# Optimization experiments

Hardware: AMD Instinct MI355X
Metric: run time of the kernel (lower is better)

## Reference

```python
import jax, jax.numpy as jnp
import numpy as np

N = 32768      # total nodes
E = 524288     # edges (avg degree 16)
HID = 256      # hidden_dim
H = 8          # heads
C = HID // H   # head dim = 32
G = 64         # graphs in batch
NPG = N // G   # nodes per graph = 512
EDIM = 2       # edge feature dim
NEG_SLOPE = 0.2  # PyG GATv2 default


def setup_inputs():
    key = jax.random.key(0)
    ks = jax.random.split(key, 12)
    s = 0.05
    return dict(
        x=jax.random.normal(ks[0], (N, HID), jnp.float32),
        edge_attr=jax.random.normal(ks[1], (E, EDIM), jnp.float32),
        # GATv2Conv params
        W_l=jax.random.normal(ks[2], (HID, HID), jnp.float32) * s,
        b_l=jnp.zeros((HID,), jnp.float32),
        W_r=jax.random.normal(ks[3], (HID, HID), jnp.float32) * s,
        b_r=jnp.zeros((HID,), jnp.float32),
        W_e=jax.random.normal(ks[4], (EDIM, HID), jnp.float32) * s,
        att=jax.random.normal(ks[5], (H, C), jnp.float32) * s,
        bias_gat=jnp.zeros((HID,), jnp.float32),
        # MultiheadAttention params (torch packed qkv layout)
        in_proj_w=jax.random.normal(ks[6], (3 * HID, HID), jnp.float32) * s,
        in_proj_b=jnp.zeros((3 * HID,), jnp.float32),
        out_proj_w=jax.random.normal(ks[7], (HID, HID), jnp.float32) * s,
        out_proj_b=jnp.zeros((HID,), jnp.float32),
        alpha_param=jnp.array(0.5, jnp.float32),
        # FFN
        W1=jax.random.normal(ks[8], (HID, 4 * HID), jnp.float32) * s,
        b1=jnp.zeros((4 * HID,), jnp.float32),
        W2=jax.random.normal(ks[9], (4 * HID, HID), jnp.float32) * s,
        b2=jnp.zeros((HID,), jnp.float32),
        # LayerNorms
        g1=jnp.ones((HID,), jnp.float32), be1=jnp.zeros((HID,), jnp.float32),
        g2=jnp.ones((HID,), jnp.float32), be2=jnp.zeros((HID,), jnp.float32),
        g3=jnp.ones((HID,), jnp.float32), be3=jnp.zeros((HID,), jnp.float32),
        edge_index=jax.random.randint(ks[10], (2, E), 0, N, jnp.int32),
        batch=jnp.repeat(jnp.arange(G, dtype=jnp.int32), NPG),
    )


def _ln(x, g, b, eps=1e-5):
    m = jnp.mean(x, -1, keepdims=True)
    v = jnp.mean((x - m) ** 2, -1, keepdims=True)
    return (x - m) * jax.lax.rsqrt(v + eps) * g + b


def _gatv2(x, edge_index, edge_attr, W_l, b_l, W_r, b_r, W_e, att, bias_gat):
    src, dst = edge_index[0], edge_index[1]
    # PyG add_self_loops with fill_value='mean': self-loop edge_attr at node i
    # is the mean of edge_attr over edges incoming to i (0 if none).
    deg = jax.ops.segment_sum(jnp.ones((E,), x.dtype), dst, num_segments=N)
    ea_mean = jax.ops.segment_sum(edge_attr, dst, num_segments=N) / jnp.maximum(deg, 1.0)[:, None]
    loop = jnp.arange(N, dtype=src.dtype)
    src2 = jnp.concatenate([src, loop])
    dst2 = jnp.concatenate([dst, loop])
    ea2 = jnp.concatenate([edge_attr, ea_mean], axis=0)  # [E+N, 2]
    xl = (x @ W_l + b_l).reshape(N, H, C)  # source transform (messages)
    xr = (x @ W_r + b_r).reshape(N, H, C)  # target transform
    ee = (ea2 @ W_e).reshape(-1, H, C)
    e = jax.nn.leaky_relu(xl[src2] + xr[dst2] + ee, NEG_SLOPE)  # [E+N, H, C]
    score = jnp.einsum('ehc,hc->eh', e, att)  # [E+N, H]
    # scatter softmax over incoming edges of each target node
    smax = jax.lax.stop_gradient(jax.ops.segment_max(score, dst2, num_segments=N))
    ex = jnp.exp(score - smax[dst2])
    ssum = jax.ops.segment_sum(ex, dst2, num_segments=N)
    alpha = ex / ssum[dst2]  # [E+N, H]
    out = jax.ops.segment_sum(alpha[:, :, None] * xl[src2], dst2, num_segments=N)
    return out.reshape(N, HID) + bias_gat


def _mha(xg, in_proj_w, in_proj_b, out_proj_w, out_proj_b):
    # xg: [G, NPG, HID]; torch nn.MultiheadAttention (batch_first, eval mode)
    qkv = xg @ in_proj_w.T + in_proj_b
    q, k, v = jnp.split(qkv, 3, axis=-1)
    q = q.reshape(G, NPG, H, C)
    k = k.reshape(G, NPG, H, C)
    v = v.reshape(G, NPG, H, C)
    scores = jnp.einsum('gqhd,gkhd->ghqk', q, k) / jnp.sqrt(jnp.float32(C))
    p = jax.nn.softmax(scores, axis=-1)
    o = jnp.einsum('ghqk,gkhd->gqhd', p, v).reshape(G, NPG, HID)
    return o @ out_proj_w.T + out_proj_b


def reference(x, edge_attr, W_l, b_l, W_r, b_r, W_e, att, bias_gat,
              in_proj_w, in_proj_b, out_proj_w, out_proj_b, alpha_param,
              W1, b1, W2, b2, g1, be1, g2, be2, g3, be3, edge_index, batch):
    local_out = _ln(
        _gatv2(x, edge_index, edge_attr, W_l, b_l, W_r, b_r, W_e, att, bias_gat),
        g1, be1)
    # batch is sorted with equal-sized graphs -> the per-graph ragged
    # attention loop equals one batched [G, NPG, NPG] attention
    xg = x.reshape(G, NPG, HID)
    global_out = _mha(xg, in_proj_w, in_proj_b, out_proj_w, out_proj_b).reshape(N, HID)
    global_out = _ln(global_out, g2, be2)
    a = jax.nn.sigmoid(alpha_param)
    combined = a * local_out + (1.0 - a) * global_out
    ffn = jax.nn.gelu(combined @ W1 + b1, approximate=False) @ W2 + b2
    return _ln(combined + ffn, g3, be3)
```

## Files before the change

kernel.cpp:

```cpp
#include <hip/hip_runtime.h>
#include <math.h>

#define N_NODES 32768
#define E_EDGES 524288
#define HIDDEN  256
#define NPG     512
#define NGRAPH  64
#define NHEAD   8
#define CDIM    32

typedef unsigned short bf16;
typedef __attribute__((ext_vector_type(8))) short short8;
typedef __attribute__((ext_vector_type(4))) float f4;

#define AS1 __attribute__((address_space(1)))
#define AS3 __attribute__((address_space(3)))

__device__ __forceinline__ void cp16(const bf16* g, bf16* l) {
    __builtin_amdgcn_global_load_lds((AS1 const unsigned int*)(const void*)g,
                                     (AS3 unsigned int*)(void*)l, 16, 0, 0);
}

__device__ inline float bf2f(unsigned short u) {
    union { unsigned int i; float f; } v; v.i = ((unsigned int)u) << 16; return v.f;
}
__device__ inline unsigned short f2bf(float f) {
    union { float f; unsigned int i; } v; v.f = f;
    unsigned int x = v.i;
    return (unsigned short)((x + 0x7FFFu + ((x >> 16) & 1u)) >> 16);
}
__device__ inline unsigned short f2bf_trunc(float f) {
    return (unsigned short)(__float_as_uint(f) >> 16);
}
__device__ inline float4 load4(const float* p) { return *(const float4*)p; }
__device__ inline float4 load4(const bf16* p) {
    ushort4 u = *(const ushort4*)p;
    return make_float4(bf2f(u.x), bf2f(u.y), bf2f(u.z), bf2f(u.w));
}
__device__ inline void store4(float* p, float4 v) { *(float4*)p = v; }
__device__ inline void store4(bf16* p, float4 v) {
    ushort4 u; u.x = f2bf(v.x); u.y = f2bf(v.y); u.z = f2bf(v.z); u.w = f2bf(v.w);
    *(ushort4*)p = u;
}


__global__ void zero_kernel(float* deg, float* ea_sum, int* fill) {
    int i = blockIdx.x * blockDim.x + threadIdx.x;
    if (i < 2 * N_NODES) ea_sum[i] = 0.0f;
    if (i < N_NODES) { deg[i] = 0.0f; fill[i] = 0; }
}

__global__ void deg_kernel(const int* __restrict__ ei, const float* __restrict__ edge_attr,
                           float* deg, float* ea_sum) {
    int e = blockIdx.x * blockDim.x + threadIdx.x;
    if (e >= E_EDGES) return;
    int d = ei[E_EDGES + e];
    atomicAdd(&deg[d], 1.0f);
    atomicAdd(&ea_sum[2 * d + 0], edge_attr[2 * e + 0]);
    atomicAdd(&ea_sum[2 * d + 1], edge_attr[2 * e + 1]);
}

__global__ __launch_bounds__(1024) void scan_kernel(const float* __restrict__ deg, int* row_ptr) {
    __shared__ int part[1024];
    int t = threadIdx.x;
    int base = t * 32;
    int loc[32];
    int s = 0;
    #pragma unroll
    for (int j = 0; j < 32; j++) {
        loc[j] = s;
        s += (int)deg[base + j] + 1;
    }
    int mysum = s;
    part[t] = s;
    __syncthreads();
    for (int off = 1; off < 1024; off <<= 1) {
        int v = 0;
        if (t >= off) v = part[t - off];
        __syncthreads();
        part[t] += v;
        __syncthreads();
    }
    int offset = part[t] - mysum;
    #pragma unroll
    for (int j = 0; j < 32; j++) row_ptr[base + j] = offset + loc[j];
    if (t == 1023) row_ptr[N_NODES] = part[1023];
}

__global__ void fill_kernel(const int* __restrict__ ei, const float* __restrict__ edge_attr,
                            const float* __restrict__ ea_sum, const float* __restrict__ deg,
                            const int* __restrict__ row_ptr, int* fill, int4* __restrict__ erec) {
    int tid = blockIdx.x * blockDim.x + threadIdx.x;
    if (tid >= E_EDGES + N_NODES) return;
    int d, src; float a0, a1;
    if (tid < E_EDGES) {
        d = ei[E_EDGES + tid];
        src = ei[tid];
        a0 = edge_attr[2 * tid + 0];
        a1 = edge_attr[2 * tid + 1];
    } else {
        d = tid - E_EDGES;
        src = d;
        float dm = fmaxf(deg[d], 1.0f);
        a0 = ea_sum[2 * d + 0] / dm;
        a1 = ea_sum[2 * d + 1] / dm;
    }
    int pos = row_ptr[d] + atomicAdd(&fill[d], 1);
    int4 r;
    r.x = src;
    r.y = __float_as_int(a0);
    r.z = __float_as_int(a1);
    r.w = 0;
    erec[pos] = r;
}

#define QSCALE 0.25506882685716462f
__global__ void convall(const float* __restrict__ x,
                        const float* __restrict__ W_l, const float* __restrict__ W_r,
                        const float* __restrict__ W1, const float* __restrict__ W2,
                        const float* __restrict__ in_proj_w, const float* __restrict__ out_proj_w,
                        const float* __restrict__ b_l, const float* __restrict__ b_r,
                        const float* __restrict__ in_proj_b,
                        bf16* xb, bf16* wlrb, bf16* w1b, bf16* w2b,
                        bf16* wipb, bf16* wopb, float* blr, float* ipb2)
{
    int b = blockIdx.x, t = threadIdx.x;
    if (b < 8192) {
        int i = b * 256 + t;
        store4(&xb[i * 4], *(const float4*)&x[i * 4]);
    } else if (b < 8448) {
        int i = (b - 8192) * 256 + t; int k = i >> 8, n = i & 255;
        wlrb[n * 256 + k] = f2bf(W_l[i]);
    } else if (b < 8704) {
        int i = (b - 8448) * 256 + t; int k = i >> 8, n = i & 255;
        wlrb[(256 + n) * 256 + k] = f2bf(W_r[i]);
    } else if (b < 9728) {
        int i = (b - 8704) * 256 + t; int k = i >> 10, n = i & 1023;
        w1b[n * 256 + k] = f2bf(W1[i]);
    } else if (b < 10752) {
        int i = (b - 9728) * 256 + t; int k = i >> 8, n = i & 255;
        w2b[n * 1024 + k] = f2bf(W2[i]);
    } else if (b < 10944) {
        int i = (b - 10752) * 256 + t;
        float4 v = *(const float4*)&in_proj_w[i * 4];
        if (i < 16384) { v.x *= QSCALE; v.y *= QSCALE; v.z *= QSCALE; v.w *= QSCALE; }
        store4(&wipb[i * 4], v);
    } else if (b < 11008) {
        int i = (b - 10944) * 256 + t;
        store4(&wopb[i * 4], *(const float4*)&out_proj_w[i * 4]);
    } else {
        blr[t] = b_l[t]; blr[256 + t] = b_r[t];
        ipb2[t] = in_proj_b[t] * QSCALE;
        ipb2[256 + t] = in_proj_b[256 + t];
        ipb2[512 + t] = in_proj_b[512 + t];
    }
}

template <int EPI>
__global__ __launch_bounds__(256) void mfma_gemm(
    const bf16* __restrict__ A, const bf16* __restrict__ Wb,
    const float* __restrict__ bias, const bf16* __restrict__ res,
    bf16* __restrict__ C, int M, int N, int K)
{
    __shared__ bf16 lds[2 * 128 * 64];
    bf16* As = lds;
    bf16* Bs = lds + 128 * 64;
    int tid = threadIdx.x;
    int wave = tid >> 6, lane = tid & 63;
    int quad = lane >> 4, l16 = lane & 15;
    int n0 = blockIdx.x * 128, m0 = blockIdx.y * 128;
    int wm = (wave & 1) * 64, wn = (wave >> 1) * 64;

    f4 acc[4][4] = {};
    int srow = tid >> 3;
    int scol = (tid & 7) * 8;

    for (int k0 = 0; k0 < K; k0 += 64) {
        #pragma unroll
        for (int i = 0; i < 4; i++) {
            int row = i * 32 + srow;
            cp16(&A[(size_t)(m0 + row) * K + k0 + scol], &As[row * 64 + scol]);
            cp16(&Wb[(size_t)(n0 + row) * K + k0 + scol], &Bs[row * 64 + scol]);
        }
        __syncthreads();
        #pragma unroll
        for (int ks = 0; ks < 2; ks++) {
            short8 af[4], bfr[4];
            #pragma unroll
            for (int mt = 0; mt < 4; mt++)
                af[mt] = *(const short8*)&As[(wm + mt * 16 + l16) * 64 + ks * 32 + quad * 8];
            #pragma unroll
            for (int nt = 0; nt < 4; nt++)
                bfr[nt] = *(const short8*)&Bs[(wn + nt * 16 + l16) * 64 + ks * 32 + quad * 8];
            #pragma unroll
            for (int mt = 0; mt < 4; mt++)
                #pragma unroll
                for (int nt = 0; nt < 4; nt++)
                    acc[mt][nt] = __builtin_amdgcn_mfma_f32_16x16x32_bf16(
                        af[mt], bfr[nt], acc[mt][nt], 0, 0, 0);
        }
        __syncthreads();
    }

    float* epi = (float*)lds + wave * 16 * 68;
    int row = lane >> 2;
    int cb = (lane & 3) * 16;
    int gn = n0 + wn + cb;
    float bb[16];
    *(float4*)&bb[0]  = *(const float4*)&bias[gn + 0];
    *(float4*)&bb[4]  = *(const float4*)&bias[gn + 4];
    *(float4*)&bb[8]  = *(const float4*)&bias[gn + 8];
    *(float4*)&bb[12] = *(const float4*)&bias[gn + 12];

    for (int mt = 0; mt < 4; mt++) {
        #pragma unroll
        for (int nt = 0; nt < 4; nt++)
            #pragma unroll
            for (int r = 0; r < 4; r++)
                epi[(quad * 4 + r) * 68 + nt * 16 + l16] = acc[mt][nt][r];
        float vv[16];
        *(float4*)&vv[0]  = *(float4*)&epi[row * 68 + cb + 0];
        *(float4*)&vv[4]  = *(float4*)&epi[row * 68 + cb + 4];
        *(float4*)&vv[8]  = *(float4*)&epi[row * 68 + cb + 8];
        *(float4*)&vv[12] = *(float4*)&epi[row * 68 + cb + 12];
        int gm = m0 + wm + mt * 16 + row;
        #pragma unroll
        for (int j = 0; j < 16; j++) vv[j] += bb[j];
        if (EPI == 1) {
            #pragma unroll
            for (int j = 0; j < 16; j++)
                vv[j] = 0.5f * vv[j] * (1.0f + erff(vv[j] * 0.70710678118654752f));
        } else if (EPI == 4) {
            ushort rr[16];
            const bf16* rp = &res[(size_t)gm * N + gn];
            *(int4*)&rr[0] = *(const int4*)&rp[0];
            *(int4*)&rr[8] = *(const int4*)&rp[8];
            #pragma unroll
            for (int j = 0; j < 16; j++) vv[j] += bf2f(rr[j]);
            float* cf = (float*)C + (size_t)gm * N + gn;
            *(float4*)&cf[0]  = *(float4*)&vv[0];
            *(float4*)&cf[4]  = *(float4*)&vv[4];
            *(float4*)&cf[8]  = *(float4*)&vv[8];
            *(float4*)&cf[12] = *(float4*)&vv[12];
            continue;
        }
        ushort o16[16];
        #pragma unroll
        for (int j = 0; j < 16; j++) o16[j] = f2bf(vv[j]);
        bf16* cp;
        if (EPI == 3) {
            bf16* dst = (gn < 256) ? C : (bf16*)res;
            int goff = (gn < 256) ? gn : gn - 256;
            cp = &dst[(size_t)gm * 256 + goff];
        } else {
            cp = &C[(size_t)gm * N + gn];
        }
        *(int4*)&cp[0] = *(int4*)&o16[0];
        *(int4*)&cp[8] = *(int4*)&o16[8];
    }
}

__global__ __launch_bounds__(256) void attn_mfma(
    const bf16* __restrict__ qkv, bf16* __restrict__ attnout)
{
    __shared__ bf16 Ks[128 * 40];
    __shared__ bf16 Vt[32 * 136];
    __shared__ bf16 Pb[4 * 64 * 40];

    int b = blockIdx.x;
    int g = b >> 4, h = (b >> 1) & 7, hlf = b & 1;
    int tid = threadIdx.x;
    int wave = tid >> 6, lane = tid & 63;
    int quad = lane >> 4, l16 = lane & 15;
    int qbase = hlf * 256 + wave * 64;
    bf16* Pw = &Pb[wave * 64 * 40];

    short8 qf[4];
    #pragma unroll
    for (int mt = 0; mt < 4; mt++) {
        size_t node = (size_t)(g * NPG + qbase + mt * 16 + l16);
        qf[mt] = *(const short8*)&qkv[node * 768 + h * CDIM + quad * 8];
    }

    f4 oacc[4][2] = {};
    float lacc[4][4] = {};

    for (int c = 0; c < 4; c++) {
        int kk0 = c * 128;
        __syncthreads();
        #pragma unroll
        for (int i = 0; i < 2; i++) {
            int idx = i * 256 + tid;
            int key = idx >> 2, kc = (idx & 3) * 8;
            *(int4*)&Ks[key * 40 + kc] =
                *(const int4*)&qkv[(size_t)(g * NPG + kk0 + key) * 768 + 256 + h * CDIM + kc];
        }
        {
            int key = tid >> 1, dblk = (tid & 1) * 16;
            ushort tmp[16];
            const bf16* vp = &qkv[(size_t)(g * NPG + kk0 + key) * 768 + 512 + h * CDIM + dblk];
            *(int4*)&tmp[0] = *(const int4*)&vp[0];
            *(int4*)&tmp[8] = *(const int4*)&vp[8];
            #pragma unroll
            for (int j = 0; j < 16; j++) Vt[(dblk + j) * 136 + key] = tmp[j];
        }
        __syncthreads();

        for (int sub = 0; sub < 4; sub++) {
            int ks0 = sub * 32;
            short8 kf[2];
            #pragma unroll
            for (int nt = 0; nt < 2; nt++)
                kf[nt] = *(const short8*)&Ks[(ks0 + nt * 16 + l16) * 40 + quad * 8];
            #pragma unroll
            for (int mt = 0; mt < 4; mt++) {
                #pragma unroll
                for (int nt = 0; nt < 2; nt++) {
                    f4 z = {0.f, 0.f, 0.f, 0.f};
                    f4 s = __builtin_amdgcn_mfma_f32_16x16x32_bf16(qf[mt], kf[nt], z, 0, 0, 0);
                    #pragma unroll
                    for (int r = 0; r < 4; r++) {
                        float p = exp2f(s[r]);
                        lacc[mt][r] += p;
                        Pw[(mt * 16 + quad * 4 + r) * 40 + nt * 16 + l16] = f2bf_trunc(p);
                    }
                }
            }
            short8 vf[2];
            #pragma unroll
            for (int dt = 0; dt < 2; dt++)
                vf[dt] = *(const short8*)&Vt[(dt * 16 + l16) * 136 + ks0 + quad * 8];
            #pragma unroll
            for (int mt = 0; mt < 4; mt++) {
                short8 pf = *(const short8*)&Pw[(mt * 16 + l16) * 40 + quad * 8];
                #pragma unroll
                for (int dt = 0; dt < 2; dt++)
                    oacc[mt][dt] = __builtin_amdgcn_mfma_f32_16x16x32_bf16(
                        pf, vf[dt], oacc[mt][dt], 0, 0, 0);
            }
        }
    }

    #pragma unroll
    for (int mt = 0; mt < 4; mt++)
        #pragma unroll
        for (int r = 0; r < 4; r++) {
            float l = lacc[mt][r];
            l += __shfl_xor(l, 1);
            l += __shfl_xor(l, 2);
            l += __shfl_xor(l, 4);
            l += __shfl_xor(l, 8);
            lacc[mt][r] = l;
        }

    #pragma unroll
    for (int mt = 0; mt < 4; mt++) {
        #pragma unroll
        for (int dt = 0; dt < 2; dt++) {
            #pragma unroll
            for (int r = 0; r < 4; r++) {
                float v = oacc[mt][dt][r] / lacc[mt][r];
                size_t node = (size_t)(g * NPG + qbase + mt * 16 + quad * 4 + r);
                attnout[node * HIDDEN + h * CDIM + dt * 16 + l16] = f2bf(v);
            }
        }
    }
}

__device__ __forceinline__ void fetchrec(
    int i, int re, int node, const int4* __restrict__ erec,
    int& s, float& a0, float& a1)
{
    if (i < re) {
        int4 r = erec[i];
        s = r.x; a0 = __int_as_float(r.y); a1 = __int_as_float(r.z);
    } else {
        s = node; a0 = 0.f; a1 = 0.f;
    }
}

__global__ __launch_bounds__(256) void gat_kernel(
    const bf16* __restrict__ xl, const bf16* __restrict__ xr,
    const int* __restrict__ row_ptr, const int4* __restrict__ erec,
    const float* __restrict__ W_e, const float* __restrict__ att,
    const float* __restrict__ bias_gat,
    const float* __restrict__ g1, const float* __restrict__ be1,
    bf16* __restrict__ out)
{
    __shared__ float pacc[2][260];
    __shared__ float plsum[2][64];
    int wave = threadIdx.x >> 6;
    int lane = threadIdx.x & 63;
    int nloc = wave >> 1, half = wave & 1;
    int node = blockIdx.x * 2 + nloc;
    int cb = lane * 4;

    float4 xr4 = load4(&xr[(size_t)node * 256 + cb]);
    float4 we0 = *(const float4*)&W_e[cb];
    float4 we1 = *(const float4*)&W_e[HIDDEN + cb];
    float4 at4 = *(const float4*)&att[cb];

    int rs = row_ptr[node], re = row_ptr[node + 1];

    float lsum = 0.f;
    float acc0 = 0.f, acc1 = 0.f, acc2 = 0.f, acc3 = 0.f;

    int i0 = rs + half;
    int s0, s1, s2;
    float a00, a01, a10, a11, a20, a21;
    fetchrec(i0,     re, node, erec, s0, a00, a01);
    fetchrec(i0 + 2, re, node, erec, s1, a10, a11);
    fetchrec(i0 + 4, re, node, erec, s2, a20, a21);
    ushort4 xu0 = *(const ushort4*)&xl[(size_t)s0 * 256 + cb];
    ushort4 xu1 = *(const ushort4*)&xl[(size_t)s1 * 256 + cb];

    for (int i = i0; i < re; i += 2) {
        int s3; float a30, a31;
        fetchrec(i + 6, re, node, erec, s3, a30, a31);
        ushort4 xu2 = *(const ushort4*)&xl[(size_t)s2 * 256 + cb];

        float4 xl4 = make_float4(bf2f(xu0.x), bf2f(xu0.y), bf2f(xu0.z), bf2f(xu0.w));
        float t, p = 0.f;
        t = xl4.x + xr4.x + a00 * we0.x + a01 * we1.x; t = (t > 0.f) ? t : 0.2f * t; p += t * at4.x;
        t = xl4.y + xr4.y + a00 * we0.y + a01 * we1.y; t = (t > 0.f) ? t : 0.2f * t; p += t * at4.y;
        t = xl4.z + xr4.z + a00 * we0.z + a01 * we1.z; t = (t > 0.f) ? t : 0.2f * t; p += t * at4.z;
        t = xl4.w + xr4.w + a00 * we0.w + a01 * we1.w; t = (t > 0.f) ? t : 0.2f * t; p += t * at4.w;
        p += __shfl_xor(p, 1);
        p += __shfl_xor(p, 2);
        p += __shfl_xor(p, 4);
        float w = __expf(p);
        lsum += w;
        acc0 += w * xl4.x; acc1 += w * xl4.y; acc2 += w * xl4.z; acc3 += w * xl4.w;

        s0 = s1; a00 = a10; a01 = a11; xu0 = xu1;
        s1 = s2; a10 = a20; a11 = a21; xu1 = xu2;
        s2 = s3; a20 = a30; a21 = a31;
    }

    if (half) {
        plsum[nloc][lane] = lsum;
        pacc[nloc][cb + 0] = acc0; pacc[nloc][cb + 1] = acc1;
        pacc[nloc][cb + 2] = acc2; pacc[nloc][cb + 3] = acc3;
    }
    __syncthreads();
    if (!half) {
        lsum += plsum[nloc][lane];
        acc0 += pacc[nloc][cb + 0]; acc1 += pacc[nloc][cb + 1];
        acc2 += pacc[nloc][cb + 2]; acc3 += pacc[nloc][cb + 3];

        float inv = 1.0f / lsum;
        float v0 = acc0 * inv + bias_gat[cb + 0];
        float v1 = acc1 * inv + bias_gat[cb + 1];
        float v2 = acc2 * inv + bias_gat[cb + 2];
        float v3 = acc3 * inv + bias_gat[cb + 3];

        float s = v0 + v1 + v2 + v3;
        #pragma unroll
        for (int m = 1; m < 64; m <<= 1) s += __shfl_xor(s, m);
        float mean = s * (1.0f / 256.0f);
        float d0 = v0 - mean, d1 = v1 - mean, d2 = v2 - mean, d3 = v3 - mean;
        float sq = d0 * d0 + d1 * d1 + d2 * d2 + d3 * d3;
        #pragma unroll
        for (int m = 1; m < 64; m <<= 1) sq += __shfl_xor(sq, m);
        float rstd = rsqrtf(sq * (1.0f / 256.0f) + 1e-5f);
        float4 o;
        o.x = d0 * rstd * g1[cb + 0] + be1[cb + 0];
        o.y = d1 * rstd * g1[cb + 1] + be1[cb + 1];
        o.z = d2 * rstd * g1[cb + 2] + be1[cb + 2];
        o.w = d3 * rstd * g1[cb + 3] + be1[cb + 3];
        store4(&out[(size_t)node * HIDDEN + cb], o);
    }
}

__global__ __launch_bounds__(256) void combine_kernel(
    const bf16* __restrict__ gout, const bf16* __restrict__ localout,
    const float* __restrict__ alpha_p,
    const float* __restrict__ g2, const float* __restrict__ be2,
    bf16* __restrict__ combined)
{
    int wave = threadIdx.x >> 6;
    int lane = threadIdx.x & 63;
    int node = blockIdx.x * 4 + wave;
    int cb = lane * 4;
    float4 gv = load4(&gout[(size_t)node * HIDDEN + cb]);
    float s = gv.x + gv.y + gv.z + gv.w;
    #pragma unroll
    for (int m = 1; m < 64; m <<= 1) s += __shfl_xor(s, m);
    float mean = s * (1.0f / 256.0f);
    float d0 = gv.x - mean, d1 = gv.y - mean, d2 = gv.z - mean, d3 = gv.w - mean;
    float sq = d0 * d0 + d1 * d1 + d2 * d2 + d3 * d3;
    #pragma unroll
    for (int m = 1; m < 64; m <<= 1) sq += __shfl_xor(sq, m);
    float rstd = rsqrtf(sq * (1.0f / 256.0f) + 1e-5f);
    float n0 = d0 * rstd * g2[cb + 0] + be2[cb + 0];
    float n1 = d1 * rstd * g2[cb + 1] + be2[cb + 1];
    float n2 = d2 * rstd * g2[cb + 2] + be2[cb + 2];
    float n3 = d3 * rstd * g2[cb + 3] + be2[cb + 3];
    float a = 1.0f / (1.0f + __expf(-alpha_p[0]));
    float4 lv = load4(&localout[(size_t)node * HIDDEN + cb]);
    float4 o;
    o.x = a * lv.x + (1.0f - a) * n0;
    o.y = a * lv.y + (1.0f - a) * n1;
    o.z = a * lv.z + (1.0f - a) * n2;
    o.w = a * lv.w + (1.0f - a) * n3;
    store4(&combined[(size_t)node * HIDDEN + cb], o);
}

__global__ __launch_bounds__(256) void finalln_kernel(
    float* __restrict__ out,
    const float* __restrict__ g3, const float* __restrict__ be3)
{
    int wave = threadIdx.x >> 6;
    int lane = threadIdx.x & 63;
    int node = blockIdx.x * 4 + wave;
    int cb = lane * 4;
    float4 v = *(const float4*)&out[(size_t)node * HIDDEN + cb];
    float s = v.x + v.y + v.z + v.w;
    #pragma unroll
    for (int m = 1; m < 64; m <<= 1) s += __shfl_xor(s, m);
    float mean = s * (1.0f / 256.0f);
    float d0 = v.x - mean, d1 = v.y - mean, d2 = v.z - mean, d3 = v.w - mean;
    float sq = d0 * d0 + d1 * d1 + d2 * d2 + d3 * d3;
    #pragma unroll
    for (int m = 1; m < 64; m <<= 1) sq += __shfl_xor(sq, m);
    float rstd = rsqrtf(sq * (1.0f / 256.0f) + 1e-5f);
    float4 o;
    o.x = d0 * rstd * g3[cb + 0] + be3[cb + 0];
    o.y = d1 * rstd * g3[cb + 1] + be3[cb + 1];
    o.z = d2 * rstd * g3[cb + 2] + be3[cb + 2];
    o.w = d3 * rstd * g3[cb + 3] + be3[cb + 3];
    *(float4*)&out[(size_t)node * HIDDEN + cb] = o;
}

extern "C" void kernel_launch(void* const* d_in, const int* in_sizes, int n_in,
                              void* d_out, int out_size, void* d_ws, size_t ws_size,
                              hipStream_t stream) {
    const float* x          = (const float*)d_in[0];
    const float* edge_attr  = (const float*)d_in[1];
    const float* W_l        = (const float*)d_in[2];
    const float* b_l        = (const float*)d_in[3];
    const float* W_r        = (const float*)d_in[4];
    const float* b_r        = (const float*)d_in[5];
    const float* W_e        = (const float*)d_in[6];
    const float* att        = (const float*)d_in[7];
    const float* bias_gat   = (const float*)d_in[8];
    const float* in_proj_w  = (const float*)d_in[9];
    const float* in_proj_b  = (const float*)d_in[10];
    const float* out_proj_w = (const float*)d_in[11];
    const float* out_proj_b = (const float*)d_in[12];
    const float* alpha_p    = (const float*)d_in[13];
    const float* W1         = (const float*)d_in[14];
    const float* b1         = (const float*)d_in[15];
    const float* W2         = (const float*)d_in[16];
    const float* b2         = (const float*)d_in[17];
    const float* g1  = (const float*)d_in[18];
    const float* be1 = (const float*)d_in[19];
    const float* g2  = (const float*)d_in[20];
    const float* be2 = (const float*)d_in[21];
    const float* g3  = (const float*)d_in[22];
    const float* be3 = (const float*)d_in[23];
    const int* edge_index = (const int*)d_in[24];

    char* base = (char*)d_ws;
    const size_t MB = 1024 * 1024;
    const size_t KB = 1024;
    float* deg     = (float*)(base + 0);
    float* ea_sum  = (float*)(base + 131072);
    int*   fill    = (int*)  (base + 393216);
    int*   row_ptr = (int*)  (base + 524288);
    bf16* wlrb = (bf16*)(base + 3 * MB);
    bf16* wipb = (bf16*)(base + 3 * MB + 256 * KB);
    bf16* wopb = (bf16*)(base + 3 * MB + 640 * KB);
    bf16* w1b  = (bf16*)(base + 3 * MB + 768 * KB);
    bf16* w2b  = (bf16*)(base + 3 * MB + 1280 * KB);
    float* blr  = (float*)(base + 5 * MB);
    float* ipb2 = (float*)(base + 5 * MB + 4 * KB);
    bf16* xb       = (bf16*)(base + 8 * MB);
    bf16* qkv      = (bf16*)(base + 24 * MB);
    bf16* attnout  = (bf16*)(base + 72 * MB);
    bf16* gout     = (bf16*)(base + 24 * MB);
    bf16* xl       = (bf16*)(base + 40 * MB);
    bf16* xr       = (bf16*)(base + 56 * MB);
    bf16* localout = (bf16*)(base + 72 * MB);
    bf16* combined = (bf16*)(base + 8 * MB);
    bf16* h1       = (bf16*)(base + 24 * MB);
    int4* erec     = (int4*)(base + 88 * MB);
    float* out = (float*)d_out;

    zero_kernel<<<(2 * N_NODES + 255) / 256, 256, 0, stream>>>(deg, ea_sum, fill);
    deg_kernel<<<E_EDGES / 256, 256, 0, stream>>>(edge_index, edge_attr, deg, ea_sum);
    scan_kernel<<<1, 1024, 0, stream>>>(deg, row_ptr);
    fill_kernel<<<(E_EDGES + N_NODES + 255) / 256, 256, 0, stream>>>(
        edge_index, edge_attr, ea_sum, deg, row_ptr, fill, erec);

    convall<<<11009, 256, 0, stream>>>(x, W_l, W_r, W1, W2, in_proj_w, out_proj_w,
                                       b_l, b_r, in_proj_b,
                                       xb, wlrb, w1b, w2b, wipb, wopb, blr, ipb2);

    mfma_gemm<0><<<dim3(6, 256), 256, 0, stream>>>(
        xb, wipb, ipb2, (const bf16*)nullptr, qkv, N_NODES, 768, 256);
    attn_mfma<<<NGRAPH * NHEAD * 2, 256, 0, stream>>>(qkv, attnout);
    mfma_gemm<0><<<dim3(2, 256), 256, 0, stream>>>(
        attnout, wopb, out_proj_b, (const bf16*)nullptr, gout, N_NODES, 256, 256);

    mfma_gemm<3><<<dim3(4, 256), 256, 0, stream>>>(
        xb, wlrb, blr, (const bf16*)xr, xl, N_NODES, 512, 256);
    gat_kernel<<<N_NODES / 2, 256, 0, stream>>>(
        xl, xr, row_ptr, erec, W_e, att, bias_gat, g1, be1, localout);

    combine_kernel<<<N_NODES / 4, 256, 0, stream>>>(
        gout, localout, alpha_p, g2, be2, combined);

    mfma_gemm<1><<<dim3(8, 256), 256, 0, stream>>>(
        combined, w1b, b1, (const bf16*)nullptr, h1, N_NODES, 1024, 256);
    mfma_gemm<4><<<dim3(2, 256), 256, 0, stream>>>(
        h1, w2b, b2, combined, (bf16*)out, N_NODES, 256, 1024);

    finalln_kernel<<<N_NODES / 4, 256, 0, stream>>>(out, g3, be3);
}
```

Measured before the change: 588.5 us.

## Fuse QKV and GAT projection GEMMs into one wide GEMM, trim gather prefetch depth

Concatenates the in_proj weights with W_l and W_r into a single 1280-wide weight matrix and bias, so one GEMM reads x once and writes qkv, xl and xr through a three-way split epilogue. The GAT kernel launch moves earlier, and workspace buffers are remapped so outputs that are still live do not alias. The GAT edge loop's software prefetch is cut from three edges ahead to two, which reduces register pressure at the cost of less latency hiding. A single larger GEMM launch removes one kernel launch and a second pass over x.

```diff
diff --git a/kernel.cpp b/kernel.cpp
--- a/kernel.cpp
+++ b/kernel.cpp
@@ -121,38 +121,43 @@
                         const float* __restrict__ in_proj_w, const float* __restrict__ out_proj_w,
                         const float* __restrict__ b_l, const float* __restrict__ b_r,
                         const float* __restrict__ in_proj_b,
-                        bf16* xb, bf16* wlrb, bf16* w1b, bf16* w2b,
-                        bf16* wipb, bf16* wopb, float* blr, float* ipb2)
+                        bf16* xb, bf16* wcat, bf16* w1b, bf16* w2b,
+                        bf16* wopb, float* bcat)
 {
     int b = blockIdx.x, t = threadIdx.x;
     if (b < 8192) {
         int i = b * 256 + t;
         store4(&xb[i * 4], *(const float4*)&x[i * 4]);
-    } else if (b < 8448) {
-        int i = (b - 8192) * 256 + t; int k = i >> 8, n = i & 255;
-        wlrb[n * 256 + k] = f2bf(W_l[i]);
-    } else if (b < 8704) {
-        int i = (b - 8448) * 256 + t; int k = i >> 8, n = i & 255;
-        wlrb[(256 + n) * 256 + k] = f2bf(W_r[i]);
-    } else if (b < 9728) {
-        int i = (b - 8704) * 256 + t; int k = i >> 10, n = i & 1023;
+    } else if (b < 8960) {
+        int i = (b - 8192) * 256 + t;
+        float v = in_proj_w[i];
+        if (i < 65536) v *= QSCALE;
+        wcat[i] = f2bf(v);
+    } else if (b < 9216) {
+        int i = (b - 8960) * 256 + t; int k = i >> 8, n = i & 255;
+        wcat[(768 + n) * 256 + k] = f2bf(W_l[i]);
+    } else if (b < 9472) {
+        int i = (b - 9216) * 256 + t; int k = i >> 8, n = i & 255;
+        wcat[(1024 + n) * 256 + k] = f2bf(W_r[i]);
+    } else if (b < 10496) {
+        int i = (b - 9472) * 256 + t; int k = i >> 10, n = i & 1023;
         w1b[n * 256 + k] = f2bf(W1[i]);
-    } else if (b < 10752) {
-        int i = (b - 9728) * 256 + t; int k = i >> 8, n = i & 255;
+    } else if (b < 11520) {
+        int i = (b - 10496) * 256 + t; int k = i >> 8, n = i & 255;
         w2b[n * 1024 + k] = f2bf(W2[i]);
-    } else if (b < 10944) {
-        int i = (b - 10752) * 256 + t;
-        float4 v = *(const float4*)&in_proj_w[i * 4];
-        if (i < 16384) { v.x *= QSCALE; v.y *= QSCALE; v.z *= QSCALE; v.w *= QSCALE; }
-        store4(&wipb[i * 4], v);
-    } else if (b < 11008) {
-        int i = (b - 10944) * 256 + t;
+    } else if (b < 11584) {
+        int i = (b - 11520) * 256 + t;
         store4(&wopb[i * 4], *(const float4*)&out_proj_w[i * 4]);
     } else {
-        blr[t] = b_l[t]; blr[256 + t] = b_r[t];
-        ipb2[t] = in_proj_b[t] * QSCALE;
-        ipb2[256 + t] = in_proj_b[256 + t];
-        ipb2[512 + t] = in_proj_b[512 + t];
+        #pragma unroll
+        for (int j = 0; j < 5; j++) {
+            int idx = j * 256 + t;
+            float v;
+            if (idx < 768) { v = in_proj_b[idx]; if (idx < 256) v *= QSCALE; }
+            else if (idx < 1024) v = b_l[idx - 768];
+            else v = b_r[idx - 1024];
+            bcat[idx] = v;
+        }
     }
 }
 
@@ -160,7 +165,7 @@
 __global__ __launch_bounds__(256) void mfma_gemm(
     const bf16* __restrict__ A, const bf16* __restrict__ Wb,
     const float* __restrict__ bias, const bf16* __restrict__ res,
-    bf16* __restrict__ C, int M, int N, int K)
+    bf16* __restrict__ C, int M, int N, int K, bf16* __restrict__ d2)
 {
     __shared__ bf16 lds[2 * 128 * 64];
     bf16* As = lds;
@@ -248,10 +253,14 @@
         #pragma unroll
         for (int j = 0; j < 16; j++) o16[j] = f2bf(vv[j]);
         bf16* cp;
-        if (EPI == 3) {
-            bf16* dst = (gn < 256) ? C : (bf16*)res;
-            int goff = (gn < 256) ? gn : gn - 256;
-            cp = &dst[(size_t)gm * 256 + goff];
+        if (EPI == 5) {
+            if (gn < 768) {
+                cp = &C[(size_t)gm * 768 + gn];
+            } else if (gn < 1024) {
+                cp = &((bf16*)res)[(size_t)gm * 256 + (gn - 768)];
+            } else {
+                cp = &d2[(size_t)gm * 256 + (gn - 1024)];
+            }
         } else {
             cp = &C[(size_t)gm * N + gn];
         }
@@ -406,18 +415,15 @@
     float acc0 = 0.f, acc1 = 0.f, acc2 = 0.f, acc3 = 0.f;
 
     int i0 = rs + half;
-    int s0, s1, s2;
-    float a00, a01, a10, a11, a20, a21;
+    int s0, s1; float a00, a01, a10, a11;
     fetchrec(i0,     re, node, erec, s0, a00, a01);
     fetchrec(i0 + 2, re, node, erec, s1, a10, a11);
-    fetchrec(i0 + 4, re, node, erec, s2, a20, a21);
     ushort4 xu0 = *(const ushort4*)&xl[(size_t)s0 * 256 + cb];
-    ushort4 xu1 = *(const ushort4*)&xl[(size_t)s1 * 256 + cb];
 
     for (int i = i0; i < re; i += 2) {
-        int s3; float a30, a31;
-        fetchrec(i + 6, re, node, erec, s3, a30, a31);
-        ushort4 xu2 = *(const ushort4*)&xl[(size_t)s2 * 256 + cb];
+        int s2; float a20, a21;
+        fetchrec(i + 4, re, node, erec, s2, a20, a21);
+        ushort4 xu1 = *(const ushort4*)&xl[(size_t)s1 * 256 + cb];
 
         float4 xl4 = make_float4(bf2f(xu0.x), bf2f(xu0.y), bf2f(xu0.z), bf2f(xu0.w));
         float t, p = 0.f;
@@ -433,8 +439,7 @@
         acc0 += w * xl4.x; acc1 += w * xl4.y; acc2 += w * xl4.z; acc3 += w * xl4.w;
 
         s0 = s1; a00 = a10; a01 = a11; xu0 = xu1;
-        s1 = s2; a10 = a20; a11 = a21; xu1 = xu2;
-        s2 = s3; a20 = a30; a21 = a31;
+        s1 = s2; a10 = a20; a11 = a21;
     }
 
     if (half) {
@@ -568,23 +573,22 @@
     float* ea_sum  = (float*)(base + 131072);
     int*   fill    = (int*)  (base + 393216);
     int*   row_ptr = (int*)  (base + 524288);
-    bf16* wlrb = (bf16*)(base + 3 * MB);
-    bf16* wipb = (bf16*)(base + 3 * MB + 256 * KB);
-    bf16* wopb = (bf16*)(base + 3 * MB + 640 * KB);
-    bf16* w1b  = (bf16*)(base + 3 * MB + 768 * KB);
-    bf16* w2b  = (bf16*)(base + 3 * MB + 1280 * KB);
-    float* blr  = (float*)(base + 5 * MB);
-    float* ipb2 = (float*)(base + 5 * MB + 4 * KB);
+    bf16* wcat = (bf16*)(base + 3 * MB);
+    bf16* w1b  = (bf16*)(base + 3 * MB + 704 * KB);
+    bf16* w2b  = (bf16*)(base + 3 * MB + 1216 * KB);
+    bf16* wopb = (bf16*)(base + 3 * MB + 1728 * KB);
+    float* bcat = (float*)(base + 5 * MB);
     bf16* xb       = (bf16*)(base + 8 * MB);
     bf16* qkv      = (bf16*)(base + 24 * MB);
-    bf16* attnout  = (bf16*)(base + 72 * MB);
+    bf16* xl       = (bf16*)(base + 40 * MB);
+    bf16* attnout  = (bf16*)(base + 8 * MB);
     bf16* gout     = (bf16*)(base + 24 * MB);
-    bf16* xl       = (bf16*)(base + 40 * MB);
-    bf16* xr       = (bf16*)(base + 56 * MB);
-    bf16* localout = (bf16*)(base + 72 * MB);
-    bf16* combined = (bf16*)(base + 8 * MB);
-    bf16* h1       = (bf16*)(base + 24 * MB);
+    bf16* localout = (bf16*)(base + 40 * MB);
+    bf16* combined = (bf16*)(base + 56 * MB);
+    bf16* h1       = (bf16*)(base + 120 * MB);
     int4* erec     = (int4*)(base + 88 * MB);
+    bf16* xl_      = (bf16*)(base + 72 * MB);
+    bf16* xr_      = (bf16*)(base + 104 * MB);
     float* out = (float*)d_out;
 
     zero_kernel<<<(2 * N_NODES + 255) / 256, 256, 0, stream>>>(deg, ea_sum, fill);
@@ -593,28 +597,27 @@
     fill_kernel<<<(E_EDGES + N_NODES + 255) / 256, 256, 0, stream>>>(
         edge_index, edge_attr, ea_sum, deg, row_ptr, fill, erec);
 
-    convall<<<11009, 256, 0, stream>>>(x, W_l, W_r, W1, W2, in_proj_w, out_proj_w,
+    convall<<<11585, 256, 0, stream>>>(x, W_l, W_r, W1, W2, in_proj_w, out_proj_w,
                                        b_l, b_r, in_proj_b,
-                                       xb, wlrb, w1b, w2b, wipb, wopb, blr, ipb2);
-
-    mfma_gemm<0><<<dim3(6, 256), 256, 0, stream>>>(
-        xb, wipb, ipb2, (const bf16*)nullptr, qkv, N_NODES, 768, 256);
+                                       xb, wcat, w1b, w2b, wopb, bcat);
+
+    mfma_gemm<5><<<dim3(10, 256), 256, 0, stream>>>(
+        xb, wcat, bcat, xl_, qkv, N_NODES, 1280, 256, xr_);
+
     attn_mfma<<<NGRAPH * NHEAD * 2, 256, 0, stream>>>(qkv, attnout);
+    gat_kernel<<<N_NODES / 2, 256, 0, stream>>>(
+        xl_, xr_, row_ptr, erec, W_e, att, bias_gat, g1, be1, localout);
+
     mfma_gemm<0><<<dim3(2, 256), 256, 0, stream>>>(
-        attnout, wopb, out_proj_b, (const bf16*)nullptr, gout, N_NODES, 256, 256);
-
-    mfma_gemm<3><<<dim3(4, 256), 256, 0, stream>>>(
-        xb, wlrb, blr, (const bf16*)xr, xl, N_NODES, 512, 256);
-    gat_kernel<<<N_NODES / 2, 256, 0, stream>>>(
-        xl, xr, row_ptr, erec, W_e, att, bias_gat, g1, be1, localout);
+        attnout, wopb, out_proj_b, (const bf16*)nullptr, gout, N_NODES, 256, 256, (bf16*)nullptr);
 
     combine_kernel<<<N_NODES / 4, 256, 0, stream>>>(
         gout, localout, alpha_p, g2, be2, combined);
 
     mfma_gemm<1><<<dim3(8, 256), 256, 0, stream>>>(
-        combined, w1b, b1, (const bf16*)nullptr, h1, N_NODES, 1024, 256);
+        combined, w1b, b1, (const bf16*)nullptr, h1, N_NODES, 1024, 256, (bf16*)nullptr);
     mfma_gemm<4><<<dim3(2, 256), 256, 0, stream>>>(
-        h1, w2b, b2, combined, (bf16*)out, N_NODES, 256, 1024);
+        h1, w2b, b2, combined, (bf16*)out, N_NODES, 256, 1024, (bf16*)nullptr);
 
     finalln_kernel<<<N_NODES / 4, 256, 0, stream>>>(out, g3, be3);
 }
```

After: 579.4 us. Within noise of the previous version (-1.5%).
